# Kernel optimization log

Measured on AMD Instinct MI355X. Metric: run time of the kernel, lower is better.

## Reference

```python
import jax, jax.numpy as jnp
import numpy as np
from jax import lax

BS, L, H = 8, 2048, 1024
NH, HD = 16, 64


def setup_inputs() -> dict:
    key = jax.random.key(0)
    ks = jax.random.split(key, 4)
    s = 1.0 / np.sqrt(H)
    xav = np.sqrt(2.0 / (NH + HD))  # xavier_normal_ for ReadingHead (fan_in=HD? torch uses dims (NH,HD))
    return {
        "hidden_states": jax.random.normal(ks[0], (BS, L, H), jnp.float32),
        "K1_w": jax.random.normal(ks[1], (H, NH * HD), jnp.float32) * s,
        "K1_b": jnp.zeros((NH * HD,), jnp.float32),
        "V1_w": jax.random.normal(ks[2], (H, NH * HD), jnp.float32) * s,
        "V1_b": jnp.zeros((NH * HD,), jnp.float32),
        "bidirection_weight": jnp.full((1, 1, NH, 1, 4), 0.25, jnp.float32),
        "ReadingHead": jax.random.normal(ks[3], (NH, HD), jnp.float32) * xav,
    }


def _nearest_valid_maps(valid, L):
    # valid: [bs, L, nh] bool. Returns fm, bm: [bs, L, 2, nh] int32, matching the
    # original sequential torch loop (including its use of len_index = L-1-j for the
    # backward map's slot 0).
    bs, _, nh = valid.shape
    mask_t = jnp.moveaxis(valid, 1, 0)  # [L, bs, nh]

    def step(carry, x):
        a, b = carry
        m, v = x
        nb = jnp.where(m, a, b)
        na = jnp.where(m, v, a)
        return (na, nb), (na, nb)

    zero = jnp.zeros((bs, nh), jnp.int32)
    idx_fwd = jnp.arange(1, L, dtype=jnp.int32)
    _, (fa, fb) = lax.scan(step, (zero, zero), (mask_t[1:], idx_fwd))
    fa = jnp.concatenate([zero[None], fa], axis=0)  # [L, bs, nh]
    fb = jnp.concatenate([zero[None], fb], axis=0)

    last = jnp.full((bs, nh), L - 1, jnp.int32)
    # backward loop stores len_index = L-1-j at position j when valid
    vals_bwd = (L - 1) - jnp.arange(L - 1, dtype=jnp.int32)
    _, (ba, bb) = lax.scan(step, (last, last), (mask_t[: L - 1], vals_bwd), reverse=True)
    ba = jnp.concatenate([ba, last[None]], axis=0)
    bb = jnp.concatenate([bb, last[None]], axis=0)

    fm = jnp.stack([fa, fb], axis=2).transpose(1, 0, 2, 3)  # [bs, L, 2, nh]
    bm = jnp.stack([ba, bb], axis=2).transpose(1, 0, 2, 3)
    return fm, bm


def reference(hidden_states, K1_w, K1_b, V1_w, V1_b, bidirection_weight, ReadingHead):
    bs, length, _ = hidden_states.shape
    nh, hd = ReadingHead.shape
    K1 = jax.nn.relu(hidden_states @ K1_w + K1_b).reshape(bs, length, nh, hd)
    V1 = jax.nn.relu(hidden_states @ V1_w + V1_b).reshape(bs, length, nh, hd)
    dots = jnp.einsum('blnh,nh->bln', K1, ReadingHead)
    valid = dots > 0.5
    fm, bm = _nearest_valid_maps(valid, length)
    # gather V along sequence dim with the two nearest-valid maps
    Vf = jnp.take_along_axis(V1, fm.reshape(bs, 2 * length, nh, 1), axis=1)
    Vf = Vf.reshape(bs, length, 2, nh, hd)
    Vb = jnp.take_along_axis(V1, bm.reshape(bs, 2 * length, nh, 1), axis=1)
    Vb = Vb.reshape(bs, length, 2, nh, hd)
    # [bs, L, 4, nh, hd] -> [bs, L, nh, hd, 4], weighted sum over the 4 registers
    new_states = jnp.concatenate([Vf, Vb], axis=2).transpose(0, 1, 3, 4, 2) * bidirection_weight
    context = new_states.sum(axis=-1).reshape(bs, length, nh * hd)
    return context
```

## Files before the change

kernel.cpp:

```cpp
#include <hip/hip_runtime.h>
#include <hip/hip_bf16.h>
#include <cstdint>

#define BS 8
#define SEQ 2048
#define HDIM 1024
#define NH 16
#define HD 64
#define M_ROWS (BS * SEQ)
#define N_COLS (2 * HDIM)
#define KDIM HDIM

#define DELTA 0.025f
#define FLAG_CAP 32768

#define OFF_A      ((size_t)0)
#define OFF_BT     ((size_t)33554432)
#define OFF_FCNT   ((size_t)37748736)
#define OFF_FLIST  ((size_t)37748800)
#define OFF_BIAS   ((size_t)37879872)
#define OFF_CVH    ((size_t)41943040)
#define OFF_VALID  ((size_t)75497472)
#define OFF_MAPS   ((size_t)75759616)

typedef __attribute__((ext_vector_type(8))) __bf16 bf16x8;
typedef __attribute__((ext_vector_type(4))) float f32x4;

__device__ __forceinline__ unsigned short f2bf(float f) {
    unsigned int x = __builtin_bit_cast(unsigned int, f);
    unsigned int r = x + 0x7fffu + ((x >> 16) & 1u);
    return (unsigned short)(r >> 16);
}
__device__ __forceinline__ float bf2f(unsigned short u) {
    return __builtin_bit_cast(float, (unsigned int)u << 16);
}

__device__ __forceinline__ void g2l16(const void* gp, void* lp) {
    __builtin_amdgcn_global_load_lds(
        (__attribute__((address_space(1))) void*)(void*)gp,
        (__attribute__((address_space(3))) void*)lp, 16, 0, 0);
}

__global__ __launch_bounds__(256) void prep_kernel(const float4* __restrict__ hs4,
                                                   ushort4* __restrict__ Abf4,
                                                   const float* __restrict__ K1w,
                                                   const float* __restrict__ V1w,
                                                   unsigned short* __restrict__ Bt,
                                                   const float* __restrict__ K1b,
                                                   const float* __restrict__ V1b,
                                                   float* __restrict__ bias,
                                                   int* __restrict__ fcnt) {
    __shared__ float tile[32][33];
    const int blk = blockIdx.x;
    const int t = threadIdx.x;
    if (blk < 16384) {
        int i = blk * 256 + t;
        float4 v = hs4[i];
        ushort4 o;
        o.x = f2bf(v.x); o.y = f2bf(v.y); o.z = f2bf(v.z); o.w = f2bf(v.w);
        Abf4[i] = o;
    } else if (blk < 18432) {
        int lb = blk - 16384;
        int z = lb >> 10;
        int tk = (lb >> 5) & 31;
        int tn = lb & 31;
        const float* W = z ? V1w : K1w;
        int r = t >> 3;
        int c4 = (t & 7) * 4;
        const float4 v = *(const float4*)&W[(size_t)(tk * 32 + r) * 1024 + tn * 32 + c4];
        tile[r][c4 + 0] = v.x; tile[r][c4 + 1] = v.y;
        tile[r][c4 + 2] = v.z; tile[r][c4 + 3] = v.w;
        __syncthreads();
        int n = tn * 32 + r;
        int k = tk * 32 + c4;
        ushort4 o;
        o.x = f2bf(tile[c4 + 0][r]); o.y = f2bf(tile[c4 + 1][r]);
        o.z = f2bf(tile[c4 + 2][r]); o.w = f2bf(tile[c4 + 3][r]);
        *(ushort4*)&Bt[((size_t)z * 1024 + n) * 1024 + k] = o;
    } else {
        int i = (blk - 18432) * 256 + t;
        bias[i] = (i < 1024) ? K1b[i] : V1b[i - 1024];
        if (i == 0) *fcnt = 0;
    }
}

__global__ __launch_bounds__(512, 2) void gemm_kernel(const unsigned short* __restrict__ Abf,
                                                      const unsigned short* __restrict__ Btbf,
                                                      const float* __restrict__ bias,
                                                      const float* __restrict__ RH,
                                                      unsigned short* __restrict__ CVh,
                                                      unsigned char* __restrict__ valid,
                                                      int* __restrict__ fcnt,
                                                      int* __restrict__ flist) {
    constexpr int K = KDIM, BK = 64;
    __shared__ unsigned short As[2][256 * BK];
    __shared__ unsigned short Bs[2][256 * BK];
    const int t = threadIdx.x;
    const int wave = t >> 6, lane = t & 63;
    const int wm = wave >> 2, wn = wave & 3;
    const int l16 = lane & 15, quad = lane >> 4;
    const int sw = l16 & 7;

    const int wgid = blockIdx.y * 8 + blockIdx.x;
    const int swz = (wgid & 7) * 64 + (wgid >> 3);
    const int m0 = (swz >> 3) * 256, n0 = (swz & 7) * 256;

    f32x4 zero4 = {0.f, 0.f, 0.f, 0.f};
    f32x4 acc[8][4];
#pragma unroll
    for (int i = 0; i < 8; i++)
#pragma unroll
        for (int j = 0; j < 4; j++) acc[i][j] = zero4;

    const int rr = t >> 3;
    const int gsw = (t ^ rr) & 7;
    const unsigned short* gA = Abf + (size_t)(m0 + rr) * K + gsw * 8;
    const unsigned short* gB = Btbf + (size_t)(n0 + rr) * K + gsw * 8;
    char* lA = (char*)As + (size_t)wave * 1024;
    char* lB = (char*)Bs + (size_t)wave * 1024;

    auto stage = [&](int buf, int k0) {
        char* a = lA + buf * 32768;
        char* b = lB + buf * 32768;
#pragma unroll
        for (int i = 0; i < 4; i++) g2l16(gA + (size_t)i * 64 * K + k0, a + i * 8192);
#pragma unroll
        for (int i = 0; i < 4; i++) g2l16(gB + (size_t)i * 64 * K + k0, b + i * 8192);
    };

    auto compute = [&](int buf) {
        const unsigned short* Ab = As[buf];
        const unsigned short* Bb = Bs[buf];
#pragma unroll
        for (int h = 0; h < 2; h++) {
            const int hq = h * 4 + quad;
            bf16x8 af[8], bfr[4];
#pragma unroll
            for (int mt = 0; mt < 8; mt++)
                af[mt] = *(const bf16x8*)&Ab[(wm * 128 + mt * 16 + l16) * BK + ((hq ^ sw) << 3)];
#pragma unroll
            for (int nt = 0; nt < 4; nt++)
                bfr[nt] = *(const bf16x8*)&Bb[(wn * 64 + nt * 16 + l16) * BK + ((hq ^ sw) << 3)];
#pragma unroll
            for (int mt = 0; mt < 8; mt++)
#pragma unroll
                for (int nt = 0; nt < 4; nt++)
                    acc[mt][nt] = __builtin_amdgcn_mfma_f32_16x16x32_bf16(af[mt], bfr[nt], acc[mt][nt], 0, 0, 0);
        }
    };

    stage(0, 0);
    __syncthreads();
#pragma unroll 1
    for (int k0 = 64; k0 < 960; k0 += 128) {
        stage(1, k0);      compute(0); __syncthreads();
        stage(0, k0 + 64); compute(1); __syncthreads();
    }
    stage(1, 960); compute(0); __syncthreads();
    compute(1);

    if (n0 < HDIM) {
        const int n = (n0 >> 6) + wn;
        float rh[4], bv[4];
#pragma unroll
        for (int nt = 0; nt < 4; nt++) {
            int col = n * 64 + nt * 16 + l16;
            rh[nt] = RH[col];
            bv[nt] = bias[col];
        }
#pragma unroll
        for (int mt = 0; mt < 8; mt++) {
#pragma unroll
            for (int r = 0; r < 4; r++) {
                float p = 0.f;
#pragma unroll
                for (int nt = 0; nt < 4; nt++)
                    p += fmaxf(acc[mt][nt][r] + bv[nt], 0.f) * rh[nt];
#pragma unroll
                for (int s = 8; s >= 1; s >>= 1) p += __shfl_xor(p, s, 64);
                if (l16 == 0) {
                    int row = m0 + wm * 128 + mt * 16 + quad * 4 + r;
                    int b = row >> 11, l = row & (SEQ - 1);
                    valid[((size_t)b * NH + n) * SEQ + l] = (p > 0.5f) ? 1 : 0;
                    if (fabsf(p - 0.5f) < DELTA) {
                        int idx = atomicAdd(fcnt, 1);
                        if (idx < FLAG_CAP) flist[idx] = row * NH + n;
                    }
                }
            }
        }
    } else {
        const int nv0 = n0 - HDIM;
        const int head = (nv0 >> 6) + wn;
        const int b = m0 >> 11;
        const int l0 = (m0 & (SEQ - 1)) + wm * 128 + quad * 4;
        unsigned short* plane = CVh + ((size_t)(b * NH + head)) * SEQ * HD;
#pragma unroll
        for (int mt = 0; mt < 8; mt++) {
#pragma unroll
            for (int nt = 0; nt < 4; nt++) {
                const int hd = nt * 16 + l16;
                const float bvv = bias[HDIM + nv0 + wn * 64 + hd];
#pragma unroll
                for (int r = 0; r < 4; r++)
                    plane[(size_t)(l0 + mt * 16 + r) * HD + hd] = f2bf(fmaxf(acc[mt][nt][r] + bvv, 0.f));
            }
        }
    }
}

__global__ __launch_bounds__(256) void refine_kernel(const float* __restrict__ hs,
                                                     const float* __restrict__ K1w,
                                                     const float* __restrict__ K1b,
                                                     const float* __restrict__ RH,
                                                     const int* __restrict__ fcnt,
                                                     const int* __restrict__ flist,
                                                     unsigned char* __restrict__ valid) {
    int cnt = *fcnt;
    if (cnt > FLAG_CAP) cnt = FLAG_CAP;
    const int wave = threadIdx.x >> 6, d = threadIdx.x & 63;
    const int task = blockIdx.x * 4 + wave;
    if (task >= cnt) return;

    const int code = flist[task];
    const int n = code & (NH - 1);
    const int bl = code >> 4;
    const float* x = hs + (size_t)bl * HDIM;
    const float* wp = K1w + n * 64 + d;

    double acc0 = 0.0, acc1 = 0.0, acc2 = 0.0, acc3 = 0.0;
    for (int k = 0; k < KDIM; k += 32) {
        float w[32];
#pragma unroll
        for (int u = 0; u < 32; u++)
            w[u] = wp[(size_t)(k + u) * 1024];
        float4 xv[8];
#pragma unroll
        for (int u = 0; u < 8; u++)
            xv[u] = *(const float4*)(x + k + u * 4);
#pragma unroll
        for (int u = 0; u < 8; u++) {
            acc0 += (double)xv[u].x * (double)w[u * 4 + 0];
            acc1 += (double)xv[u].y * (double)w[u * 4 + 1];
            acc2 += (double)xv[u].z * (double)w[u * 4 + 2];
            acc3 += (double)xv[u].w * (double)w[u * 4 + 3];
        }
    }
    double k1 = ((acc0 + acc1) + (acc2 + acc3)) + (double)K1b[n * 64 + d];
    if (k1 < 0.0) k1 = 0.0;
    double contrib = k1 * (double)RH[n * 64 + d];
#pragma unroll
    for (int s = 32; s >= 1; s >>= 1) contrib += __shfl_xor(contrib, s, 64);
    if (d == 0) {
        int b = bl >> 11, l = bl & (SEQ - 1);
        valid[((size_t)b * NH + n) * SEQ + l] = (contrib > 0.5) ? 1 : 0;
    }
}

__global__ __launch_bounds__(64) void scan_kernel(const unsigned char* __restrict__ valid,
                                                  ushort4* __restrict__ maps) {
    int bn = blockIdx.x;
    int b = bn >> 4, n = bn & (NH - 1);
    int lane = threadIdx.x;
    __shared__ unsigned int summ[64];

    const unsigned char* vp = valid + (size_t)bn * SEQ + lane * 32;
    uint4 c0 = *(const uint4*)vp;
    uint4 c1 = *(const uint4*)(vp + 16);
    unsigned int wds[8] = {c0.x, c0.y, c0.z, c0.w, c1.x, c1.y, c1.z, c1.w};
    unsigned int mask = 0;
#pragma unroll
    for (int i = 0; i < 8; i++) {
#pragma unroll
        for (int j = 0; j < 4; j++)
            mask |= (((wds[i] >> (8 * j)) & 0xffu) ? 1u : 0u) << (i * 4 + j);
    }

    int cnt = 0, va = 0, vb = 0;
#pragma unroll
    for (int tt = 0; tt < 32; tt++) {
        if (mask & (1u << tt)) { vb = va; va = lane * 32 + tt; cnt++; }
    }
    summ[lane] = (unsigned)((cnt > 2 ? 2 : cnt) | (va << 2) | (vb << 13));
    __syncthreads();
    int a = 0, bb_ = 0;
    for (int tt = 0; tt < lane; tt++) {
        unsigned s = summ[tt];
        int c = s & 3, sva = (s >> 2) & 2047, svb = (s >> 13) & 2047;
        if (c >= 2) { a = sva; bb_ = svb; }
        else if (c == 1) { bb_ = a; a = sva; }
    }
    unsigned int fres[32];
#pragma unroll
    for (int tt = 0; tt < 32; tt++) {
        if (mask & (1u << tt)) { bb_ = a; a = lane * 32 + tt; }
        fres[tt] = (unsigned)a | ((unsigned)bb_ << 16);
    }
    __syncthreads();

    unsigned int maskb = mask;
    if (lane == 63) maskb &= ~(1u << 31);
    cnt = 0; va = 0; vb = 0;
#pragma unroll
    for (int tt = 31; tt >= 0; tt--) {
        if (maskb & (1u << tt)) { vb = va; va = (SEQ - 1) - (lane * 32 + tt); cnt++; }
    }
    summ[lane] = (unsigned)((cnt > 2 ? 2 : cnt) | (va << 2) | (vb << 13));
    __syncthreads();
    int a2 = SEQ - 1, b2 = SEQ - 1;
    for (int tt = 63; tt > lane; tt--) {
        unsigned s = summ[tt];
        int c = s & 3, sva = (s >> 2) & 2047, svb = (s >> 13) & 2047;
        if (c >= 2) { a2 = sva; b2 = svb; }
        else if (c == 1) { b2 = a2; a2 = sva; }
    }
#pragma unroll
    for (int tt = 31; tt >= 0; tt--) {
        int j = lane * 32 + tt;
        if (maskb & (1u << tt)) { b2 = a2; a2 = (SEQ - 1) - j; }
        unsigned f = fres[tt];
        maps[((size_t)b * SEQ + j) * NH + n] =
            make_ushort4((unsigned short)(f & 0xffffu), (unsigned short)(f >> 16),
                         (unsigned short)a2, (unsigned short)b2);
    }
}

__global__ __launch_bounds__(256) void gather_kernel(const unsigned short* __restrict__ CVh,
                                                     const ushort4* __restrict__ maps,
                                                     const float* __restrict__ bw,
                                                     float* __restrict__ out) {
    int bl = blockIdx.x;
    int t = threadIdx.x, n = t >> 4, q = t & 15;
    int b = bl >> 11;
    ushort4 m = maps[(size_t)bl * NH + n];
    const float4 w = *(const float4*)&bw[n * 4];
    const unsigned short* plane = CVh + ((size_t)(b * NH + n)) * SEQ * HD + q * 4;
    const ushort4 u0 = *(const ushort4*)&plane[(size_t)m.x * HD];
    const ushort4 u1 = *(const ushort4*)&plane[(size_t)m.y * HD];
    const ushort4 u2 = *(const ushort4*)&plane[(size_t)m.z * HD];
    const ushort4 u3 = *(const ushort4*)&plane[(size_t)m.w * HD];
    float4 o;
    o.x = w.x * bf2f(u0.x) + w.y * bf2f(u1.x) + w.z * bf2f(u2.x) + w.w * bf2f(u3.x);
    o.y = w.x * bf2f(u0.y) + w.y * bf2f(u1.y) + w.z * bf2f(u2.y) + w.w * bf2f(u3.y);
    o.z = w.x * bf2f(u0.z) + w.y * bf2f(u1.z) + w.z * bf2f(u2.z) + w.w * bf2f(u3.z);
    o.w = w.x * bf2f(u0.w) + w.y * bf2f(u1.w) + w.z * bf2f(u2.w) + w.w * bf2f(u3.w);
    *(float4*)&out[(size_t)bl * (NH * HD) + n * 64 + q * 4] = o;
}

extern "C" void kernel_launch(void* const* d_in, const int* in_sizes, int n_in,
                              void* d_out, int out_size, void* d_ws, size_t ws_size,
                              hipStream_t stream) {
    (void)in_sizes; (void)n_in; (void)out_size; (void)ws_size;
    const float* hs  = (const float*)d_in[0];
    const float* K1w = (const float*)d_in[1];
    const float* K1b = (const float*)d_in[2];
    const float* V1w = (const float*)d_in[3];
    const float* V1b = (const float*)d_in[4];
    const float* bw  = (const float*)d_in[5];
    const float* RH  = (const float*)d_in[6];
    float* out = (float*)d_out;
    char* ws = (char*)d_ws;

    unsigned short* Abf  = (unsigned short*)(ws + OFF_A);
    unsigned short* Btbf = (unsigned short*)(ws + OFF_BT);
    int* fcnt = (int*)(ws + OFF_FCNT);
    int* flist = (int*)(ws + OFF_FLIST);
    float* bias  = (float*)(ws + OFF_BIAS);
    unsigned short* CVh = (unsigned short*)(ws + OFF_CVH);
    unsigned char* valid = (unsigned char*)(ws + OFF_VALID);
    ushort4* maps = (ushort4*)(ws + OFF_MAPS);

    prep_kernel<<<18440, 256, 0, stream>>>((const float4*)hs, (ushort4*)Abf,
                                           K1w, V1w, Btbf, K1b, V1b, bias, fcnt);
    gemm_kernel<<<dim3(N_COLS / 256, M_ROWS / 256), 512, 0, stream>>>(
        Abf, Btbf, bias, RH, CVh, valid, fcnt, flist);
    refine_kernel<<<FLAG_CAP / 4, 256, 0, stream>>>(
        hs, K1w, K1b, RH, fcnt, flist, valid);
    scan_kernel<<<BS * NH, 64, 0, stream>>>(valid, maps);
    gather_kernel<<<BS * SEQ, 256, 0, stream>>>(CVh, maps, bw, out);
}
```

Before: 384.4 us.

## Interleave fine-grained global-to-LDS loads with MFMA quarter tiles in GEMM

Restructures the GEMM main loop so each K-tile is split into four MFMA quarter-steps, each preceded by two async global-to-LDS loads, gated by partial vmcnt waits and bare barriers instead of full __syncthreads. MFMA blocks are wrapped in s_setprio to favour compute issue. The goal is to overlap memory loads with matrix math at finer granularity and cut full-drain stalls. It relies on delicate vmcnt accounting. The last iteration reloads K offset 960 into a buffer that is never consumed, wasting some bandwidth.

```diff
diff --git a/kernel.cpp b/kernel.cpp
--- a/kernel.cpp
+++ b/kernel.cpp
@@ -92,9 +92,9 @@
                                                       unsigned char* __restrict__ valid,
                                                       int* __restrict__ fcnt,
                                                       int* __restrict__ flist) {
-    constexpr int K = KDIM, BK = 64;
-    __shared__ unsigned short As[2][256 * BK];
-    __shared__ unsigned short Bs[2][256 * BK];
+    constexpr int K = KDIM;
+    __shared__ unsigned short As[2][256 * 64];
+    __shared__ unsigned short Bs[2][256 * 64];
     const int t = threadIdx.x;
     const int wave = t >> 6, lane = t & 63;
     const int wm = wave >> 2, wn = wave & 3;
@@ -119,45 +119,58 @@
     char* lA = (char*)As + (size_t)wave * 1024;
     char* lB = (char*)Bs + (size_t)wave * 1024;
 
-    auto stage = [&](int buf, int k0) {
-        char* a = lA + buf * 32768;
-        char* b = lB + buf * 32768;
-#pragma unroll
-        for (int i = 0; i < 4; i++) g2l16(gA + (size_t)i * 64 * K + k0, a + i * 8192);
-#pragma unroll
-        for (int i = 0; i < 4; i++) g2l16(gB + (size_t)i * 64 * K + k0, b + i * 8192);
+    auto stA = [&](int buf, int i, int kn) {
+        g2l16(gA + (size_t)i * 64 * K + kn, lA + buf * 32768 + i * 8192);
     };
-
-    auto compute = [&](int buf) {
+    auto stB = [&](int buf, int i, int kn) {
+        g2l16(gB + (size_t)i * 64 * K + kn, lB + buf * 32768 + i * 8192);
+    };
+
+    auto quad4 = [&](int buf, int mh, int kk4) {
         const unsigned short* Ab = As[buf];
         const unsigned short* Bb = Bs[buf];
-#pragma unroll
-        for (int h = 0; h < 2; h++) {
-            const int hq = h * 4 + quad;
-            bf16x8 af[8], bfr[4];
-#pragma unroll
-            for (int mt = 0; mt < 8; mt++)
-                af[mt] = *(const bf16x8*)&Ab[(wm * 128 + mt * 16 + l16) * BK + ((hq ^ sw) << 3)];
+        const int g = (((kk4 + quad) ^ sw) << 3);
+        bf16x8 af[4], bfr[4];
+#pragma unroll
+        for (int mt = 0; mt < 4; mt++)
+            af[mt] = *(const bf16x8*)&Ab[(wm * 128 + mh * 64 + mt * 16 + l16) * 64 + g];
+#pragma unroll
+        for (int nt = 0; nt < 4; nt++)
+            bfr[nt] = *(const bf16x8*)&Bb[(wn * 64 + nt * 16 + l16) * 64 + g];
+        __builtin_amdgcn_s_setprio(1);
+#pragma unroll
+        for (int mt = 0; mt < 4; mt++)
 #pragma unroll
             for (int nt = 0; nt < 4; nt++)
-                bfr[nt] = *(const bf16x8*)&Bb[(wn * 64 + nt * 16 + l16) * BK + ((hq ^ sw) << 3)];
-#pragma unroll
-            for (int mt = 0; mt < 8; mt++)
-#pragma unroll
-                for (int nt = 0; nt < 4; nt++)
-                    acc[mt][nt] = __builtin_amdgcn_mfma_f32_16x16x32_bf16(af[mt], bfr[nt], acc[mt][nt], 0, 0, 0);
-        }
+                acc[mh * 4 + mt][nt] =
+                    __builtin_amdgcn_mfma_f32_16x16x32_bf16(af[mt], bfr[nt], acc[mh * 4 + mt][nt], 0, 0, 0);
+        __builtin_amdgcn_s_setprio(0);
     };
 
-    stage(0, 0);
-    __syncthreads();
+#define VW4 asm volatile("s_waitcnt vmcnt(4)" ::: "memory")
+#define BARR __builtin_amdgcn_s_barrier()
+
+    stB(0, 0, 0); stB(0, 1, 0); stB(0, 2, 0); stB(0, 3, 0);
+    stA(0, 0, 0); stA(0, 2, 0); stA(0, 1, 0); stA(0, 3, 0);
+
 #pragma unroll 1
-    for (int k0 = 64; k0 < 960; k0 += 128) {
-        stage(1, k0);      compute(0); __syncthreads();
-        stage(0, k0 + 64); compute(1); __syncthreads();
-    }
-    stage(1, 960); compute(0); __syncthreads();
-    compute(1);
+    for (int tp = 0; tp < 8; ++tp) {
+        const int ka = tp * 128 + 64;
+        const int kb = (tp == 7) ? 960 : tp * 128 + 128;
+        stB(1, 0, ka); stB(1, 1, ka); VW4; BARR; quad4(0, 0, 0);
+        stB(1, 2, ka); stB(1, 3, ka); VW4; BARR; quad4(0, 1, 0);
+        stA(1, 0, ka); stA(1, 2, ka); VW4; BARR; quad4(0, 0, 4);
+        stA(1, 1, ka); stA(1, 3, ka); VW4; BARR; quad4(0, 1, 4);
+        BARR;
+        stB(0, 0, kb); stB(0, 1, kb); VW4; BARR; quad4(1, 0, 0);
+        stB(0, 2, kb); stB(0, 3, kb); VW4; BARR; quad4(1, 1, 0);
+        stA(0, 0, kb); stA(0, 2, kb); VW4; BARR; quad4(1, 0, 4);
+        stA(0, 1, kb); stA(0, 3, kb); VW4; BARR; quad4(1, 1, 4);
+        BARR;
+    }
+    asm volatile("s_waitcnt vmcnt(0)" ::: "memory");
+#undef VW4
+#undef BARR
 
     if (n0 < HDIM) {
         const int n = (n0 >> 6) + wn;
```

New measurement: 383.5 us. Within noise of the previous version (-0.2%).
